# Performance work log

Hardware: AMD Instinct MI355X
Metric: run time of the kernel (lower is better)

## Reference

```python
import jax, jax.numpy as jnp
import numpy as np

N_HEADS = 16
QUANT_BITS = 8


def fake_quantize(x, bits=QUANT_BITS):
    # Global max-abs fake quantization with STE (grad = identity).
    if bits >= 16:
        return x
    max_val = jnp.max(jnp.abs(x))
    half_levels = jnp.asarray(2.0 ** (bits - 1), x.dtype)
    q = jnp.round(x / max_val * half_levels) / half_levels * max_val
    q = jnp.where(max_val > 0, q, x)
    return x + jax.lax.stop_gradient(q - x)


def qat_linear(x, W, b):
    # torch nn.Linear: y = x @ W.T + b, with fake-quant on input and output.
    xq = fake_quantize(x)
    y = jnp.einsum('bsd,od->bso', xq, W) + b
    return fake_quantize(y)


def setup_inputs() -> dict:
    key = jax.random.key(0)
    ks = jax.random.split(key, 9)
    d = 1024
    B, S = 2, 2048
    scale = 1.0 / np.sqrt(d)
    return {
        'x': jax.random.normal(ks[0], (B, S, d), jnp.float32),
        'Wq': jax.random.normal(ks[1], (d, d), jnp.float32) * scale,
        'bq': jax.random.normal(ks[2], (d,), jnp.float32) * 0.01,
        'Wk': jax.random.normal(ks[3], (d, d), jnp.float32) * scale,
        'bk': jax.random.normal(ks[4], (d,), jnp.float32) * 0.01,
        'Wv': jax.random.normal(ks[5], (d, d), jnp.float32) * scale,
        'bv': jax.random.normal(ks[6], (d,), jnp.float32) * 0.01,
        'Wo': jax.random.normal(ks[7], (d, d), jnp.float32) * scale,
        'bo': jax.random.normal(ks[8], (d,), jnp.float32) * 0.01,
    }


def reference(x, Wq, bq, Wk, bk, Wv, bv, Wo, bo):
    B, S, d_model = x.shape
    d_k = d_model // N_HEADS

    def split_heads(t):  # [B,S,D] -> [B,H,S,dk]
        return t.reshape(B, S, N_HEADS, d_k).transpose(0, 2, 1, 3)

    Q = split_heads(qat_linear(x, Wq, bq))
    K = split_heads(qat_linear(x, Wk, bk))
    V = split_heads(qat_linear(x, Wv, bv))

    scores = jnp.einsum('bhqd,bhkd->bhqk', Q, K) / jnp.sqrt(jnp.asarray(d_k, x.dtype))
    attn = jax.nn.softmax(scores, axis=-1)  # dropout = identity (deterministic ref)
    out = jnp.einsum('bhqk,bhkd->bhqd', attn, V)
    out = out.transpose(0, 2, 1, 3).reshape(B, S, d_model)
    return qat_linear(out, Wo, bo)
```

## Files before the change

kernel.cpp:

```cpp
#include <hip/hip_runtime.h>
#include <math.h>

#define DMODEL 1024
#define SEQ    2048
#define NELEM  4194304
#define N4     (NELEM / 4)

typedef __attribute__((ext_vector_type(8))) short short8;
typedef __attribute__((ext_vector_type(4))) short short4v;
typedef __attribute__((ext_vector_type(4))) float f32x4;

#if __has_builtin(__builtin_amdgcn_exp2f)
#define EXP2(x) __builtin_amdgcn_exp2f(x)
#else
#define EXP2(x) exp2f(x)
#endif

__device__ __forceinline__ void gl2lds16(const unsigned short* g, unsigned short* l) {
    __builtin_amdgcn_global_load_lds(
        (const __attribute__((address_space(1))) unsigned int*)g,
        (__attribute__((address_space(3))) unsigned int*)l,
        16, 0, 0);
}

__device__ __forceinline__ float fq(float x, float m) {
    float t = x / m * 128.0f;
    float r = rintf(t);
    float q = r * 0.0078125f * m;
    return (m > 0.0f) ? q : x;
}
__device__ __forceinline__ unsigned short f2bf(float f) {
    unsigned int u = __float_as_uint(f);
    u += 0x7FFFu + ((u >> 16) & 1u);
    return (unsigned short)(u >> 16);
}
__device__ __forceinline__ float bf2f(unsigned short h) {
    return __uint_as_float(((unsigned int)h) << 16);
}
__device__ __forceinline__ unsigned short qint(float x, float m) {
    float i = rintf(x / m * 128.0f);
    return (unsigned short)(__float_as_uint(i) >> 16);
}

__device__ __forceinline__ void block_max_atomic(float v, float* red, unsigned int* slot) {
    const int t = threadIdx.x;
    red[t] = v;
    __syncthreads();
    #pragma unroll
    for (int s = 128; s > 0; s >>= 1) {
        if (t < s) red[t] = fmaxf(red[t], red[t + s]);
        __syncthreads();
    }
    if (t == 0) atomicMax(slot, __float_as_uint(red[0]));
}

__global__ __launch_bounds__(256) void wsplit_absmax(
    const float* __restrict__ W0, const float* __restrict__ W1,
    const float* __restrict__ W2, const float* __restrict__ W3,
    unsigned short* __restrict__ H0, unsigned short* __restrict__ L0,
    unsigned short* __restrict__ H1, unsigned short* __restrict__ L1,
    unsigned short* __restrict__ H2, unsigned short* __restrict__ L2,
    unsigned short* __restrict__ H3, unsigned short* __restrict__ L3,
    const float* __restrict__ x, int n4, unsigned int* __restrict__ slot) {
    __shared__ float red[256];
    const int z = blockIdx.y;
    if (z == 4) {
        float m = 0.0f;
        const float4* x4 = (const float4*)x;
        for (int i = blockIdx.x * 256 + threadIdx.x; i < n4; i += gridDim.x * 256) {
            float4 v = x4[i];
            m = fmaxf(m, fmaxf(fmaxf(fabsf(v.x), fabsf(v.y)), fmaxf(fabsf(v.z), fabsf(v.w))));
        }
        block_max_atomic(m, red, slot);
        return;
    }
    const float* W = (z == 0) ? W0 : (z == 1) ? W1 : (z == 2) ? W2 : W3;
    unsigned short* H = (z == 0) ? H0 : (z == 1) ? H1 : (z == 2) ? H2 : H3;
    unsigned short* L = (z == 0) ? L0 : (z == 1) ? L1 : (z == 2) ? L2 : L3;
    const int i = blockIdx.x * 256 + threadIdx.x;
    float4 w = ((const float4*)W)[i];
    ushort4 h, l;
    h.x = f2bf(w.x); l.x = f2bf(w.x - bf2f(h.x));
    h.y = f2bf(w.y); l.y = f2bf(w.y - bf2f(h.y));
    h.z = f2bf(w.z); l.z = f2bf(w.z - bf2f(h.z));
    h.w = f2bf(w.w); l.w = f2bf(w.w - bf2f(h.w));
    ((ushort4*)H)[i] = h;
    ((ushort4*)L)[i] = l;
}

__global__ __launch_bounds__(256) void quant_int_kernel(const float* __restrict__ src,
                                                        unsigned short* __restrict__ dst,
                                                        const unsigned int* __restrict__ slot,
                                                        int n4) {
    const float m = __uint_as_float(*slot);
    const float4* s4 = (const float4*)src;
    for (int i = blockIdx.x * 256 + threadIdx.x; i < n4; i += gridDim.x * 256) {
        float4 v = s4[i];
        ushort4 o;
        o.x = qint(v.x, m); o.y = qint(v.y, m); o.z = qint(v.z, m); o.w = qint(v.w, m);
        ((ushort4*)dst)[i] = o;
    }
}

__global__ __launch_bounds__(256) void quant_out_kernel(float* __restrict__ Y,
                                                        const unsigned int* __restrict__ slot,
                                                        int n4) {
    const float m = __uint_as_float(*slot);
    float4* y4 = (float4*)Y;
    for (int i = blockIdx.x * 256 + threadIdx.x; i < n4; i += gridDim.x * 256) {
        float4 v = y4[i];
        v.x = fq(v.x, m); v.y = fq(v.y, m); v.z = fq(v.z, m); v.w = fq(v.w, m);
        y4[i] = v;
    }
}

__global__ __launch_bounds__(256) void quantK_vtrans(
    const float* __restrict__ Kraw, unsigned short* __restrict__ Ki,
    const unsigned int* __restrict__ slotK,
    const float* __restrict__ Vraw, unsigned short* __restrict__ Vti,
    const unsigned int* __restrict__ slotV, int n4) {
    __shared__ float tile[64][65];
    if (blockIdx.y == 0) {
        const float m = __uint_as_float(*slotK);
        const float4* s4 = (const float4*)Kraw;
        for (int i = blockIdx.x * 256 + threadIdx.x; i < n4; i += gridDim.x * 256) {
            float4 v = s4[i];
            ushort4 o;
            o.x = qint(v.x, m); o.y = qint(v.y, m); o.z = qint(v.z, m); o.w = qint(v.w, m);
            ((ushort4*)Ki)[i] = o;
        }
        return;
    }
    const float mv = __uint_as_float(*slotV);
    const int t = threadIdx.x;
    const int s0 = (blockIdx.x & 31) << 6;
    const int bh = blockIdx.x >> 5;
    const int b = bh >> 4, h = bh & 15;
    const int rr = t >> 4;
    const int cc = (t & 15) << 2;
    #pragma unroll
    for (int rep = 0; rep < 4; rep++) {
        int srow = rep * 16 + rr;
        float4 v = *(const float4*)&Vraw[(size_t)b * SEQ * DMODEL + (size_t)(s0 + srow) * DMODEL + h * 64 + cc];
        tile[srow][cc + 0] = v.x; tile[srow][cc + 1] = v.y;
        tile[srow][cc + 2] = v.z; tile[srow][cc + 3] = v.w;
    }
    __syncthreads();
    #pragma unroll
    for (int rep = 0; rep < 4; rep++) {
        int drow = rep * 16 + rr;
        ushort4 o;
        o.x = qint(tile[cc + 0][drow], mv);
        o.y = qint(tile[cc + 1][drow], mv);
        o.z = qint(tile[cc + 2][drow], mv);
        o.w = qint(tile[cc + 3][drow], mv);
        *(ushort4*)&Vti[(size_t)bh * 64 * SEQ + (size_t)drow * SEQ + s0 + cc] = o;
    }
}

template<int BN>
__global__ __launch_bounds__(256) void gemm_mfma(
    const unsigned short* __restrict__ Ai, const unsigned int* __restrict__ mSlot,
    const unsigned short* __restrict__ Wh0, const unsigned short* __restrict__ Wl0,
    const float* __restrict__ b0, float* __restrict__ O0, unsigned int* __restrict__ s0,
    const unsigned short* __restrict__ Wh1, const unsigned short* __restrict__ Wl1,
    const float* __restrict__ b1, float* __restrict__ O1, unsigned int* __restrict__ s1,
    const unsigned short* __restrict__ Wh2, const unsigned short* __restrict__ Wl2,
    const float* __restrict__ b2, float* __restrict__ O2, unsigned int* __restrict__ s2) {
    constexpr int NI = BN / 32;
    __shared__ __align__(16) unsigned short As[128 * 32];
    __shared__ __align__(16) unsigned short Bh[BN * 32];
    __shared__ __align__(16) unsigned short Bl[BN * 32];
    __shared__ float red[256];

    const int z = blockIdx.z;
    const unsigned short* Wh = (z == 0) ? Wh0 : (z == 1) ? Wh1 : Wh2;
    const unsigned short* Wl = (z == 0) ? Wl0 : (z == 1) ? Wl1 : Wl2;
    const float* bias = (z == 0) ? b0 : (z == 1) ? b1 : b2;
    float* O = (z == 0) ? O0 : (z == 1) ? O1 : O2;
    unsigned int* slotOut = (z == 0) ? s0 : (z == 1) ? s1 : s2;

    const float mA = __uint_as_float(*mSlot);
    const int t = threadIdx.x;
    const int lane = t & 63, w = t >> 6;
    const int ml = lane & 15, qd = lane >> 4;
    const int wm = w & 1, wn = w >> 1;
    const int m0 = blockIdx.y << 7;
    const int n0 = blockIdx.x * BN;

    const int lr = lane >> 2;
    const int lc = (lane & 3) << 3;
    const unsigned short* Asrc = Ai + (size_t)(m0 + w * 32 + lr) * DMODEL + lc;
    const unsigned short* Hsrc = Wh + (size_t)(n0 + w * (BN / 4) + lr) * DMODEL + lc;
    const unsigned short* Lsrc = Wl + (size_t)(n0 + w * (BN / 4) + lr) * DMODEL + lc;
    unsigned short* Adst = &As[(w * 32) * 32];
    unsigned short* Hdst = &Bh[(w * (BN / 4)) * 32];
    unsigned short* Ldst = &Bl[(w * (BN / 4)) * 32];

    f32x4 acc[4][NI];
    #pragma unroll
    for (int mi = 0; mi < 4; mi++)
        #pragma unroll
        for (int ni = 0; ni < NI; ni++) acc[mi][ni] = (f32x4){0.f, 0.f, 0.f, 0.f};

    for (int k0 = 0; k0 < DMODEL; k0 += 32) {
        __syncthreads();
        gl2lds16(Asrc + k0,               Adst);
        gl2lds16(Asrc + k0 + 16 * DMODEL, Adst + 16 * 32);
        if constexpr (BN == 128) {
            gl2lds16(Hsrc + k0,               Hdst);
            gl2lds16(Hsrc + k0 + 16 * DMODEL, Hdst + 16 * 32);
            gl2lds16(Lsrc + k0,               Ldst);
            gl2lds16(Lsrc + k0 + 16 * DMODEL, Ldst + 16 * 32);
        } else {
            gl2lds16(Hsrc + k0, Hdst);
            gl2lds16(Lsrc + k0, Ldst);
        }
        __syncthreads();

        short8 af[4];
        #pragma unroll
        for (int mi = 0; mi < 4; mi++)
            af[mi] = *(const short8*)&As[(wm * 64 + mi * 16 + ml) * 32 + qd * 8];
        #pragma unroll
        for (int ni = 0; ni < NI; ni++) {
            short8 bh = *(const short8*)&Bh[(wn * (BN / 2) + ni * 16 + ml) * 32 + qd * 8];
            short8 bl = *(const short8*)&Bl[(wn * (BN / 2) + ni * 16 + ml) * 32 + qd * 8];
            #pragma unroll
            for (int mi = 0; mi < 4; mi++) {
                acc[mi][ni] = __builtin_amdgcn_mfma_f32_16x16x32_bf16(af[mi], bh, acc[mi][ni], 0, 0, 0);
                acc[mi][ni] = __builtin_amdgcn_mfma_f32_16x16x32_bf16(af[mi], bl, acc[mi][ni], 0, 0, 0);
            }
        }
    }

    const float s = mA * 0.0078125f;
    float lmax = 0.0f;
    #pragma unroll
    for (int ni = 0; ni < NI; ni++) {
        const int col = n0 + wn * (BN / 2) + ni * 16 + ml;
        const float bc = bias[col];
        #pragma unroll
        for (int mi = 0; mi < 4; mi++) {
            #pragma unroll
            for (int r = 0; r < 4; r++) {
                int row = m0 + wm * 64 + mi * 16 + qd * 4 + r;
                float v = acc[mi][ni][r] * s + bc;
                lmax = fmaxf(lmax, fabsf(v));
                O[row * DMODEL + col] = v;
            }
        }
    }
    block_max_atomic(lmax, red, slotOut);
}

__global__ __launch_bounds__(256) void attn_mfma(
    const float* __restrict__ Qraw, const unsigned short* __restrict__ Ki,
    const unsigned short* __restrict__ Vti, const unsigned int* __restrict__ slots,
    float* __restrict__ Out, unsigned int* __restrict__ moSlot) {
    __shared__ __align__(16) unsigned short Ks[2][64 * 72];
    __shared__ __align__(16) unsigned short Vt[2][64 * 72];
    __shared__ float red[256];
    union U8 { short8 v; unsigned short u[8]; };
    union U4 { short4v v; unsigned short u[4]; };

    const int t = threadIdx.x;
    const int lane = t & 63, w = t >> 6;
    const int ml = lane & 15, qd = lane >> 4;
    const int q0 = blockIdx.x << 7;
    const int bh = blockIdx.y;
    const int b = bh >> 4, h = bh & 15;
    const float mq = __uint_as_float(slots[1]);
    const float mk = __uint_as_float(slots[2]);
    const float mv = __uint_as_float(slots[3]);
    const float c2 = (mq * 0.0078125f) * (mk * 0.0078125f) * 0.125f * 1.4426950408889634f;
    const int baseQ = b * SEQ * DMODEL + h * 64;
    const int qgA = q0 + w * 32 + ml;
    const int qgB = qgA + 16;

    short8 bq[2][2];
    #pragma unroll
    for (int g = 0; g < 2; g++) {
        const float* src = Qraw + baseQ + (size_t)(g ? qgB : qgA) * DMODEL + qd * 8;
        #pragma unroll
        for (int c = 0; c < 2; c++) {
            float4 v0 = *(const float4*)(src + c * 32);
            float4 v1 = *(const float4*)(src + c * 32 + 4);
            U8 tmp;
            tmp.u[0] = qint(v0.x, mq); tmp.u[1] = qint(v0.y, mq);
            tmp.u[2] = qint(v0.z, mq); tmp.u[3] = qint(v0.w, mq);
            tmp.u[4] = qint(v1.x, mq); tmp.u[5] = qint(v1.y, mq);
            tmp.u[6] = qint(v1.z, mq); tmp.u[7] = qint(v1.w, mq);
            bq[g][c] = tmp.v;
        }
    }

    f32x4 oacc[2][4];
    #pragma unroll
    for (int g = 0; g < 2; g++)
        #pragma unroll
        for (int i = 0; i < 4; i++) oacc[g][i] = (f32x4){0.f, 0.f, 0.f, 0.f};
    float mrun[2] = {-INFINITY, -INFINITY}, lrun[2] = {0.f, 0.f};

    const int sr = t >> 2;
    const int sc = (t & 3) << 4;
    const unsigned short* kstage = Ki + baseQ + (size_t)sr * DMODEL + sc;
    const unsigned short* vstage = Vti + (size_t)bh * 64 * SEQ + (size_t)sr * SEQ + sc;

    {
        short8 a = *(const short8*)kstage;
        short8 bb = *(const short8*)(kstage + 8);
        short8 c = *(const short8*)vstage;
        short8 d = *(const short8*)(vstage + 8);
        *(short8*)&Ks[0][sr * 72 + sc] = a;
        *(short8*)&Ks[0][sr * 72 + sc + 8] = bb;
        *(short8*)&Vt[0][sr * 72 + sc] = c;
        *(short8*)&Vt[0][sr * 72 + sc + 8] = d;
    }
    __syncthreads();

    for (int it = 0; it < 32; it++) {
        const int cur = it & 1;
        short8 nk0, nk1, nv0, nv1;
        if (it < 31) {
            const size_t ko = (size_t)(it + 1) * 64;
            nk0 = *(const short8*)(kstage + ko * DMODEL);
            nk1 = *(const short8*)(kstage + ko * DMODEL + 8);
            nv0 = *(const short8*)(vstage + ko);
            nv1 = *(const short8*)(vstage + ko + 8);
        }

        f32x4 sacc[2][4];
        #pragma unroll
        for (int tau = 0; tau < 4; tau++) {
            short8 a0 = *(const short8*)&Ks[cur][(tau * 16 + ml) * 72 + qd * 8];
            short8 a1 = *(const short8*)&Ks[cur][(tau * 16 + ml) * 72 + 32 + qd * 8];
            #pragma unroll
            for (int g = 0; g < 2; g++) {
                f32x4 z4 = (f32x4){0.f, 0.f, 0.f, 0.f};
                z4 = __builtin_amdgcn_mfma_f32_16x16x32_bf16(a0, bq[g][0], z4, 0, 0, 0);
                sacc[g][tau] = __builtin_amdgcn_mfma_f32_16x16x32_bf16(a1, bq[g][1], z4, 0, 0, 0);
            }
        }

        float alpha[2];
        short4v phi[2][4], plo[2][4];
        #pragma unroll
        for (int g = 0; g < 2; g++) {
            float tmax = fmaxf(fmaxf(fmaxf(sacc[g][0][0], sacc[g][0][1]), fmaxf(sacc[g][0][2], sacc[g][0][3])),
                               fmaxf(fmaxf(sacc[g][1][0], sacc[g][1][1]), fmaxf(sacc[g][1][2], sacc[g][1][3])));
            tmax = fmaxf(tmax, fmaxf(fmaxf(fmaxf(sacc[g][2][0], sacc[g][2][1]), fmaxf(sacc[g][2][2], sacc[g][2][3])),
                                     fmaxf(fmaxf(sacc[g][3][0], sacc[g][3][1]), fmaxf(sacc[g][3][2], sacc[g][3][3]))));
            tmax = fmaxf(tmax, __shfl_xor(tmax, 16));
            tmax = fmaxf(tmax, __shfl_xor(tmax, 32));
            const float mnew = fmaxf(mrun[g], tmax);
            alpha[g] = EXP2((mrun[g] - mnew) * c2);
            const float mc = mnew * c2;
            float ls = 0.0f;
            #pragma unroll
            for (int tau = 0; tau < 4; tau++) {
                U4 hh, ll;
                #pragma unroll
                for (int r = 0; r < 4; r++) {
                    float pv = EXP2(sacc[g][tau][r] * c2 - mc);
                    ls += pv;
                    unsigned int u = __float_as_uint(pv);
                    unsigned int uh = (u + 0x8000u) & 0xFFFF0000u;
                    hh.u[r] = (unsigned short)(uh >> 16);
                    float lf = pv - __uint_as_float(uh);
                    ll.u[r] = (unsigned short)(__float_as_uint(lf) >> 16);
                }
                phi[g][tau] = hh.v;
                plo[g][tau] = ll.v;
            }
            ls += __shfl_xor(ls, 16);
            ls += __shfl_xor(ls, 32);
            lrun[g] = lrun[g] * alpha[g] + ls;
            mrun[g] = mnew;
        }

        #pragma unroll
        for (int g = 0; g < 2; g++)
            #pragma unroll
            for (int i = 0; i < 4; i++) {
                oacc[g][i][0] *= alpha[g]; oacc[g][i][1] *= alpha[g];
                oacc[g][i][2] *= alpha[g]; oacc[g][i][3] *= alpha[g];
            }

        #pragma unroll
        for (int td = 0; td < 4; td++) {
            #pragma unroll
            for (int tau = 0; tau < 4; tau++) {
                short4v av = *(const short4v*)&Vt[cur][(td * 16 + ml) * 72 + tau * 16 + qd * 4];
                #pragma unroll
                for (int g = 0; g < 2; g++) {
                    oacc[g][td] = __builtin_amdgcn_mfma_f32_16x16x16bf16_1k(av, phi[g][tau], oacc[g][td], 0, 0, 0);
                    oacc[g][td] = __builtin_amdgcn_mfma_f32_16x16x16bf16_1k(av, plo[g][tau], oacc[g][td], 0, 0, 0);
                }
            }
        }

        if (it < 31) {
            *(short8*)&Ks[cur ^ 1][sr * 72 + sc] = nk0;
            *(short8*)&Ks[cur ^ 1][sr * 72 + sc + 8] = nk1;
            *(short8*)&Vt[cur ^ 1][sr * 72 + sc] = nv0;
            *(short8*)&Vt[cur ^ 1][sr * 72 + sc + 8] = nv1;
        }
        __syncthreads();
    }

    float lmax = 0.0f;
    #pragma unroll
    for (int g = 0; g < 2; g++) {
        const float inv = (mv * 0.0078125f) / lrun[g];
        const int qg = g ? qgB : qgA;
        #pragma unroll
        for (int td = 0; td < 4; td++) {
            float4 o;
            o.x = oacc[g][td][0] * inv;
            o.y = oacc[g][td][1] * inv;
            o.z = oacc[g][td][2] * inv;
            o.w = oacc[g][td][3] * inv;
            lmax = fmaxf(lmax, fmaxf(fmaxf(fabsf(o.x), fabsf(o.y)), fmaxf(fabsf(o.z), fabsf(o.w))));
            *(float4*)&Out[baseQ + (size_t)qg * DMODEL + td * 16 + qd * 4] = o;
        }
    }
    block_max_atomic(lmax, red, moSlot);
}

extern "C" void kernel_launch(void* const* d_in, const int* in_sizes, int n_in,
                              void* d_out, int out_size, void* d_ws, size_t ws_size,
                              hipStream_t stream) {
    const float* x  = (const float*)d_in[0];
    const float* Wq = (const float*)d_in[1];
    const float* bq = (const float*)d_in[2];
    const float* Wk = (const float*)d_in[3];
    const float* bk = (const float*)d_in[4];
    const float* Wv = (const float*)d_in[5];
    const float* bv = (const float*)d_in[6];
    const float* Wo = (const float*)d_in[7];
    const float* bo = (const float*)d_in[8];
    float* out = (float*)d_out;

    const size_t MB = 1024 * 1024;
    unsigned int* slots = (unsigned int*)d_ws;
    char* p = (char*)d_ws + 256;
    unsigned short* WqH = (unsigned short*)(p + 0 * MB);
    unsigned short* WqL = (unsigned short*)(p + 2 * MB);
    unsigned short* WkH = (unsigned short*)(p + 4 * MB);
    unsigned short* WkL = (unsigned short*)(p + 6 * MB);
    unsigned short* WvH = (unsigned short*)(p + 8 * MB);
    unsigned short* WvL = (unsigned short*)(p + 10 * MB);
    unsigned short* WoH = (unsigned short*)(p + 12 * MB);
    unsigned short* WoL = (unsigned short*)(p + 14 * MB);
    unsigned short* Xi  = (unsigned short*)(p + 16 * MB);
    float* RA  = (float*)(p + 24 * MB);
    float* RB  = (float*)(p + 40 * MB);
    unsigned short* Vti = (unsigned short*)(p + 56 * MB);
    unsigned short* Ki  = (unsigned short*)(p + 4 * MB);
    unsigned short* Oi  = (unsigned short*)RA;
    float* Qraw = out;

    hipMemsetAsync(d_ws, 0, 256, stream);

    wsplit_absmax<<<dim3(1024, 5), 256, 0, stream>>>(Wq, Wk, Wv, Wo,
        WqH, WqL, WkH, WkL, WvH, WvL, WoH, WoL, x, N4, slots + 0);
    quant_int_kernel<<<1024, 256, 0, stream>>>(x, Xi, slots + 0, N4);

    gemm_mfma<64><<<dim3(16, 32, 3), 256, 0, stream>>>(Xi, slots + 0,
        WqH, WqL, bq, Qraw, slots + 1,
        WkH, WkL, bk, RA,   slots + 2,
        WvH, WvL, bv, RB,   slots + 3);
    quantK_vtrans<<<dim3(1024, 2), 256, 0, stream>>>(RA, Ki, slots + 2,
                                                     RB, Vti, slots + 3, N4);

    attn_mfma<<<dim3(16, 32), 256, 0, stream>>>(Qraw, Ki, Vti, slots, RB, slots + 4);
    quant_int_kernel<<<1024, 256, 0, stream>>>(RB, Oi, slots + 4, N4);

    gemm_mfma<64><<<dim3(16, 32, 1), 256, 0, stream>>>(Oi, slots + 4,
        WoH, WoL, bo, out, slots + 5,
        WoH, WoL, bo, out, slots + 5,
        WoH, WoL, bo, out, slots + 5);
    quant_out_kernel<<<1024, 256, 0, stream>>>(out, slots + 5, N4);
}
```

Measured before the change: 314.2 us.

## Deepen GEMM K-step, swap grid order, use wave-level max, truncate P split

The GEMM now stages two 32-wide K slices per barrier pair (K step of 64), which halves the number of __syncthreads per tile. The block mapping is swapped so consecutive blocks walk along M and share the same weight columns. The block-wide max reduction in the GEMM and attention epilogues is replaced by a wave shuffle reduction, with one atomic per wave. The bf16 hi/lo split of the softmax probabilities now truncates the high half instead of rounding it, saving a few ALU ops, and the lo term still captures the residual.

Result: slower. 365.5 us (+16.3%).

```diff
diff --git a/kernel.cpp b/kernel.cpp
--- a/kernel.cpp
+++ b/kernel.cpp
@@ -52,6 +52,16 @@
         __syncthreads();
     }
     if (t == 0) atomicMax(slot, __float_as_uint(red[0]));
+}
+
+__device__ __forceinline__ void wave_max_atomic(float v, int lane, unsigned int* slot) {
+    v = fmaxf(v, __shfl_xor(v, 1));
+    v = fmaxf(v, __shfl_xor(v, 2));
+    v = fmaxf(v, __shfl_xor(v, 4));
+    v = fmaxf(v, __shfl_xor(v, 8));
+    v = fmaxf(v, __shfl_xor(v, 16));
+    v = fmaxf(v, __shfl_xor(v, 32));
+    if (lane == 0) atomicMax(slot, __float_as_uint(v));
 }
 
 __global__ __launch_bounds__(256) void wsplit_absmax(
@@ -168,10 +178,9 @@
     const unsigned short* __restrict__ Wh2, const unsigned short* __restrict__ Wl2,
     const float* __restrict__ b2, float* __restrict__ O2, unsigned int* __restrict__ s2) {
     constexpr int NI = BN / 32;
-    __shared__ __align__(16) unsigned short As[128 * 32];
-    __shared__ __align__(16) unsigned short Bh[BN * 32];
-    __shared__ __align__(16) unsigned short Bl[BN * 32];
-    __shared__ float red[256];
+    __shared__ __align__(16) unsigned short As[2][128 * 32];
+    __shared__ __align__(16) unsigned short Bh[2][BN * 32];
+    __shared__ __align__(16) unsigned short Bl[2][BN * 32];
 
     const int z = blockIdx.z;
     const unsigned short* Wh = (z == 0) ? Wh0 : (z == 1) ? Wh1 : Wh2;
@@ -185,17 +194,14 @@
     const int lane = t & 63, w = t >> 6;
     const int ml = lane & 15, qd = lane >> 4;
     const int wm = w & 1, wn = w >> 1;
-    const int m0 = blockIdx.y << 7;
-    const int n0 = blockIdx.x * BN;
+    const int m0 = blockIdx.x << 7;
+    const int n0 = blockIdx.y * BN;
 
     const int lr = lane >> 2;
     const int lc = (lane & 3) << 3;
     const unsigned short* Asrc = Ai + (size_t)(m0 + w * 32 + lr) * DMODEL + lc;
     const unsigned short* Hsrc = Wh + (size_t)(n0 + w * (BN / 4) + lr) * DMODEL + lc;
     const unsigned short* Lsrc = Wl + (size_t)(n0 + w * (BN / 4) + lr) * DMODEL + lc;
-    unsigned short* Adst = &As[(w * 32) * 32];
-    unsigned short* Hdst = &Bh[(w * (BN / 4)) * 32];
-    unsigned short* Ldst = &Bl[(w * (BN / 4)) * 32];
 
     f32x4 acc[4][NI];
     #pragma unroll
@@ -203,33 +209,33 @@
         #pragma unroll
         for (int ni = 0; ni < NI; ni++) acc[mi][ni] = (f32x4){0.f, 0.f, 0.f, 0.f};
 
-    for (int k0 = 0; k0 < DMODEL; k0 += 32) {
+    for (int k0 = 0; k0 < DMODEL; k0 += 64) {
         __syncthreads();
-        gl2lds16(Asrc + k0,               Adst);
-        gl2lds16(Asrc + k0 + 16 * DMODEL, Adst + 16 * 32);
-        if constexpr (BN == 128) {
-            gl2lds16(Hsrc + k0,               Hdst);
-            gl2lds16(Hsrc + k0 + 16 * DMODEL, Hdst + 16 * 32);
-            gl2lds16(Lsrc + k0,               Ldst);
-            gl2lds16(Lsrc + k0 + 16 * DMODEL, Ldst + 16 * 32);
-        } else {
-            gl2lds16(Hsrc + k0, Hdst);
-            gl2lds16(Lsrc + k0, Ldst);
+        #pragma unroll
+        for (int hb = 0; hb < 2; hb++) {
+            const int ko = k0 + hb * 32;
+            gl2lds16(Asrc + ko,               &As[hb][(w * 32) * 32]);
+            gl2lds16(Asrc + ko + 16 * DMODEL, &As[hb][(w * 32 + 16) * 32]);
+            gl2lds16(Hsrc + ko, &Bh[hb][(w * (BN / 4)) * 32]);
+            gl2lds16(Lsrc + ko, &Bl[hb][(w * (BN / 4)) * 32]);
         }
         __syncthreads();
 
-        short8 af[4];
-        #pragma unroll
-        for (int mi = 0; mi < 4; mi++)
-            af[mi] = *(const short8*)&As[(wm * 64 + mi * 16 + ml) * 32 + qd * 8];
-        #pragma unroll
-        for (int ni = 0; ni < NI; ni++) {
-            short8 bh = *(const short8*)&Bh[(wn * (BN / 2) + ni * 16 + ml) * 32 + qd * 8];
-            short8 bl = *(const short8*)&Bl[(wn * (BN / 2) + ni * 16 + ml) * 32 + qd * 8];
-            #pragma unroll
-            for (int mi = 0; mi < 4; mi++) {
-                acc[mi][ni] = __builtin_amdgcn_mfma_f32_16x16x32_bf16(af[mi], bh, acc[mi][ni], 0, 0, 0);
-                acc[mi][ni] = __builtin_amdgcn_mfma_f32_16x16x32_bf16(af[mi], bl, acc[mi][ni], 0, 0, 0);
+        #pragma unroll
+        for (int hb = 0; hb < 2; hb++) {
+            short8 af[4];
+            #pragma unroll
+            for (int mi = 0; mi < 4; mi++)
+                af[mi] = *(const short8*)&As[hb][(wm * 64 + mi * 16 + ml) * 32 + qd * 8];
+            #pragma unroll
+            for (int ni = 0; ni < NI; ni++) {
+                short8 bh = *(const short8*)&Bh[hb][(wn * (BN / 2) + ni * 16 + ml) * 32 + qd * 8];
+                short8 bl = *(const short8*)&Bl[hb][(wn * (BN / 2) + ni * 16 + ml) * 32 + qd * 8];
+                #pragma unroll
+                for (int mi = 0; mi < 4; mi++) {
+                    acc[mi][ni] = __builtin_amdgcn_mfma_f32_16x16x32_bf16(af[mi], bh, acc[mi][ni], 0, 0, 0);
+                    acc[mi][ni] = __builtin_amdgcn_mfma_f32_16x16x32_bf16(af[mi], bl, acc[mi][ni], 0, 0, 0);
+                }
             }
         }
     }
@@ -251,7 +257,7 @@
             }
         }
     }
-    block_max_atomic(lmax, red, slotOut);
+    wave_max_atomic(lmax, lane, slotOut);
 }
 
 __global__ __launch_bounds__(256) void attn_mfma(
@@ -260,7 +266,6 @@
     float* __restrict__ Out, unsigned int* __restrict__ moSlot) {
     __shared__ __align__(16) unsigned short Ks[2][64 * 72];
     __shared__ __align__(16) unsigned short Vt[2][64 * 72];
-    __shared__ float red[256];
     union U8 { short8 v; unsigned short u[8]; };
     union U4 { short4v v; unsigned short u[4]; };
 
@@ -365,8 +370,8 @@
                     float pv = EXP2(sacc[g][tau][r] * c2 - mc);
                     ls += pv;
                     unsigned int u = __float_as_uint(pv);
-                    unsigned int uh = (u + 0x8000u) & 0xFFFF0000u;
-                    hh.u[r] = (unsigned short)(uh >> 16);
+                    unsigned int uh = u & 0xFFFF0000u;
+                    hh.u[r] = (unsigned short)(u >> 16);
                     float lf = pv - __uint_as_float(uh);
                     ll.u[r] = (unsigned short)(__float_as_uint(lf) >> 16);
                 }
@@ -425,7 +430,7 @@
             *(float4*)&Out[baseQ + (size_t)qg * DMODEL + td * 16 + qd * 4] = o;
         }
     }
-    block_max_atomic(lmax, red, moSlot);
+    wave_max_atomic(lmax, lane, moSlot);
 }
 
 extern "C" void kernel_launch(void* const* d_in, const int* in_sizes, int n_in,
@@ -467,7 +472,7 @@
         WqH, WqL, WkH, WkL, WvH, WvL, WoH, WoL, x, N4, slots + 0);
     quant_int_kernel<<<1024, 256, 0, stream>>>(x, Xi, slots + 0, N4);
 
-    gemm_mfma<64><<<dim3(16, 32, 3), 256, 0, stream>>>(Xi, slots + 0,
+    gemm_mfma<64><<<dim3(32, 16, 3), 256, 0, stream>>>(Xi, slots + 0,
         WqH, WqL, bq, Qraw, slots + 1,
         WkH, WkL, bk, RA,   slots + 2,
         WvH, WvL, bv, RB,   slots + 3);
@@ -477,7 +482,7 @@
     attn_mfma<<<dim3(16, 32), 256, 0, stream>>>(Qraw, Ki, Vti, slots, RB, slots + 4);
     quant_int_kernel<<<1024, 256, 0, stream>>>(RB, Oi, slots + 4, N4);
 
-    gemm_mfma<64><<<dim3(16, 32, 1), 256, 0, stream>>>(Oi, slots + 4,
+    gemm_mfma<64><<<dim3(32, 16, 1), 256, 0, stream>>>(Oi, slots + 4,
         WoH, WoL, bo, out, slots + 5,
         WoH, WoL, bo, out, slots + 5,
         WoH, WoL, bo, out, slots + 5);
```
